# Kernel tuning notes

Measured on AMD Instinct MI355X. Metric: run time of the kernel, lower is better.

The kernel has to match this reference:

```python
import jax, jax.numpy as jnp
import numpy as np

N = 100000
E = 1600000
D_IN, D_HID, D_OUT = 128, 128, 128


def gcn_conv(x, edge_index, W, b):
    """PyG GCNConv with default symmetric normalization and added self-loops.
    out = D^{-1/2} (A + I) D^{-1/2} (x W) + b, edge weights = 1.
    """
    n = x.shape[0]
    h = x @ W                                   # [N, D_out]
    src, dst = edge_index[0], edge_index[1]     # messages flow src -> dst
    ones = jnp.ones(src.shape[0], dtype=x.dtype)
    # degree includes the self-loop (+1), computed on the target index as in PyG
    deg = jax.ops.segment_sum(ones, dst, num_segments=n) + 1.0  # [N]
    dinv = jax.lax.rsqrt(deg)                   # deg >= 1 so safe
    norm = dinv[src] * dinv[dst]                # [E]
    msg = h[src] * norm[:, None]                # [E, D_out]
    agg = jax.ops.segment_sum(msg, dst, num_segments=n)
    # self-loop contribution: norm = dinv_i * dinv_i = 1/deg_i
    out = agg + h * (dinv * dinv)[:, None] + b
    return out


def layer_norm(x, gamma, beta, eps=1e-5):
    mu = jnp.mean(x, axis=-1, keepdims=True)
    var = jnp.mean(jnp.square(x - mu), axis=-1, keepdims=True)
    return (x - mu) * jax.lax.rsqrt(var + eps) * gamma + beta


def setup_inputs() -> dict:
    key = jax.random.key(0)
    ks = jax.random.split(key, 8)
    x = jax.random.normal(ks[0], (N, D_IN), dtype=jnp.float32)
    edge_index = jax.random.randint(ks[1], (2, E), 0, N, dtype=jnp.int64)
    s1 = 1.0 / np.sqrt(D_IN)
    s2 = 1.0 / np.sqrt(D_HID)
    W1 = jax.random.uniform(ks[2], (D_IN, D_HID), jnp.float32, -s1, s1)
    b1 = jnp.zeros((D_HID,), jnp.float32)
    W2 = jax.random.uniform(ks[3], (D_HID, D_OUT), jnp.float32, -s2, s2)
    b2 = jnp.zeros((D_OUT,), jnp.float32)
    gamma = jnp.ones((D_OUT,), jnp.float32)
    beta = jnp.zeros((D_OUT,), jnp.float32)
    return {"x": x, "edge_index": edge_index, "W1": W1, "b1": b1,
            "W2": W2, "b2": b2, "gamma": gamma, "beta": beta}


def reference(x, edge_index, W1, b1, W2, b2, gamma, beta):
    h = gcn_conv(x, edge_index, W1, b1)
    h = jax.nn.relu(h)
    # dropout is identity in eval mode (deterministic reference)
    h = gcn_conv(h, edge_index, W2, b2)
    return layer_norm(h, gamma, beta)
```

## Files before the change

kernel.cpp:

```cpp
#include <hip/hip_runtime.h>


#define N_NODES 100000
#define N_EDGES 1600000
#define NBLK_N  391
#define NB      196
#define BKT_CAP 8960
#define BIN_GRID 391
#define GEMM_GRID 1563
#define MM_GRID  6250

typedef unsigned int  u32;
typedef unsigned short u16;
typedef unsigned char u8;
typedef unsigned long long u64;
typedef __attribute__((ext_vector_type(8))) short bf16x8;
typedef __attribute__((ext_vector_type(4))) float f32x4;

__device__ __forceinline__ float bflo(u32 u){ return __uint_as_float(u << 16); }
__device__ __forceinline__ float bfhi(u32 u){ return __uint_as_float(u & 0xFFFF0000u); }
__device__ __forceinline__ u32 f2b(float f){
  u32 u = __float_as_uint(f);
  return (u + 0x7FFFu + ((u >> 16) & 1u)) >> 16;
}
__device__ __forceinline__ u32 pack2(float a, float b){ return f2b(a) | (f2b(b) << 16); }
__device__ __forceinline__ u32 clampN(int s){
  u32 u = (u32)s;
  return (u < (u32)N_NODES) ? u : (u32)(N_NODES - 1);
}

__global__ __launch_bounds__(64) void detect(const int* __restrict__ ei,
                                             int* __restrict__ flags){
  int l = threadIdx.x;
  int nzodd = (ei[2 * l + 1] != 0) ? 1 : 0;
  #pragma unroll
  for (int o = 32; o > 0; o >>= 1) nzodd += __shfl_xor(nzodd, o, 64);
  if (l == 0) flags[1] = (nzodd == 0) ? 1 : 0;
}


__device__ __forceinline__ void build_wfrag(u16* wfrag, const float* __restrict__ W,
                                            int tid){
  #pragma unroll
  for (int i = 0; i < 8; ++i){
    int fid   = tid + i * 256;
    int lane  = fid & 63;
    int kb    = (fid >> 6) & 3;
    int ntile = fid >> 8;
    int n  = ntile * 16 + (lane & 15);
    int k0 = kb * 32 + (lane >> 4) * 8;
    u16 tmp[8];
    #pragma unroll
    for (int j = 0; j < 8; ++j) tmp[j] = (u16)f2b(W[(k0 + j) * 128 + n]);
    *(bf16x8*)(wfrag + (size_t)fid * 8) = *(const bf16x8*)tmp;
  }
}

__device__ __forceinline__ void gemm_tail(const u16* wfrag, const bf16x8 afrag[4],
                                          int rowbase, int lane,
                                          u16* __restrict__ Hout, int nrows){
  const int m = lane & 15, q = lane >> 4;
  f32x4 acc[8];
  #pragma unroll
  for (int n = 0; n < 8; ++n) acc[n] = (f32x4){0.f, 0.f, 0.f, 0.f};
  #pragma unroll
  for (int n = 0; n < 8; ++n){
    #pragma unroll
    for (int kb = 0; kb < 4; ++kb){
      bf16x8 bfrag = *(const bf16x8*)(wfrag + ((size_t)(n * 4 + kb) * 64 + lane) * 8);
      acc[n] = __builtin_amdgcn_mfma_f32_16x16x32_bf16(afrag[kb], bfrag, acc[n], 0, 0, 0);
    }
  }
  #pragma unroll
  for (int r = 0; r < 4; ++r){
    int orow = rowbase + q * 4 + r;
    if (orow < nrows){
      u16* Or = Hout + (size_t)orow * 128 + m;
      #pragma unroll
      for (int n = 0; n < 8; ++n) Or[n * 16] = (u16)f2b(acc[n][r]);
    }
  }
}

__device__ __forceinline__ void gemm_f32_body(u16* wfrag, const float* __restrict__ A,
                                              const float* __restrict__ W,
                                              u16* __restrict__ Hout, int nrows, int bid){
  build_wfrag(wfrag, W, threadIdx.x);
  __syncthreads();
  const int lane = threadIdx.x & 63;
  const int wv   = threadIdx.x >> 6;
  const int rowbase = bid * 64 + wv * 16;
  const int row  = rowbase + (lane & 15);
  const int rowc = (row < nrows) ? row : (nrows - 1);
  const int q    = lane >> 4;
  bf16x8 afrag[4];
  const float* Ar = A + (size_t)rowc * 128;
  #pragma unroll
  for (int kb = 0; kb < 4; ++kb){
    f32x4 p0 = *(const f32x4*)(Ar + kb * 32 + q * 8);
    f32x4 p1 = *(const f32x4*)(Ar + kb * 32 + q * 8 + 4);
    bf16x8 f;
    f[0] = (short)f2b(p0[0]); f[1] = (short)f2b(p0[1]);
    f[2] = (short)f2b(p0[2]); f[3] = (short)f2b(p0[3]);
    f[4] = (short)f2b(p1[0]); f[5] = (short)f2b(p1[1]);
    f[6] = (short)f2b(p1[2]); f[7] = (short)f2b(p1[3]);
    afrag[kb] = f;
  }
  gemm_tail(wfrag, afrag, rowbase, lane, Hout, nrows);
}


__device__ __forceinline__ void binA_body(u32* cnt ,
                                          const int* __restrict__ ei,
                                          u32* __restrict__ binned,
                                          u32* __restrict__ bucket_fill, int bb){
  u32* gbase = cnt + 256;
  u32* flagp = cnt + 512;
  const int tid = threadIdx.x;
  cnt[tid] = 0;
  if (tid < 64){
    int nz = (ei[2 * tid + 1] != 0) ? 1 : 0;
    u64 b = __ballot(nz);
    if (tid == 0) *flagp = (b == 0ull) ? 1u : 0u;
  }
  __syncthreads();
  const int i64  = (int)*flagp;
  const int base = bb * 4096;
  u32 pk[16], rk[16], bk[16];
  #pragma unroll
  for (int j = 0; j < 16; ++j){
    int e = base + tid + j * 256;
    bk[j] = 0xFFFFFFFFu;
    if (e < N_EDGES){
      int dsti = i64 ? ei[2 * N_EDGES + 2 * e] : ei[N_EDGES + e];
      int srci = i64 ? ei[2 * e]               : ei[e];
      u32 ud = clampN(dsti), us = clampN(srci);
      u32 b = ud >> 9;
      bk[j] = b;
      pk[j] = us | ((ud & 511u) << 17);
      rk[j] = atomicAdd(&cnt[b], 1u);
    }
  }
  __syncthreads();
  u32 c = cnt[tid];
  u32 old = 0;
  if (c) old = atomicAdd(&bucket_fill[tid < NB ? tid : 0], tid < NB ? c : 0u);
  gbase[tid] = old;
  __syncthreads();
  #pragma unroll
  for (int j = 0; j < 16; ++j){
    if (bk[j] != 0xFFFFFFFFu){
      u32 idx = gbase[bk[j]] + rk[j];
      if (idx < BKT_CAP) binned[(size_t)bk[j] * BKT_CAP + idx] = pk[j];
    }
  }
}


__global__ __launch_bounds__(256) void fused_gemm_bin(const float* __restrict__ A,
                                                      const float* __restrict__ W,
                                                      u16* __restrict__ Hout,
                                                      const int* __restrict__ ei,
                                                      u32* __restrict__ binned,
                                                      u32* __restrict__ bucket_fill){
  __shared__ u16 smem[16384];
  if (blockIdx.x < GEMM_GRID){
    gemm_f32_body(smem, A, W, Hout, N_NODES, blockIdx.x);
  } else {
    binA_body((u32*)smem, ei, binned, bucket_fill, blockIdx.x - GEMM_GRID);
  }
}

__global__ __launch_bounds__(256) void gemm_f32in(const float* __restrict__ A,
                                                  const float* __restrict__ W,
                                                  u16* __restrict__ Hout){
  __shared__ u16 smem[16384];
  gemm_f32_body(smem, A, W, Hout, N_NODES, blockIdx.x);
}


__global__ __launch_bounds__(256) void fill_sort(const u32* __restrict__ binned,
                                                 const u32* __restrict__ bucket_fill,
                                                 int* __restrict__ offs,
                                                 float* __restrict__ dinv,
                                                 int* __restrict__ srclist){
  __shared__ u32 cnt[512];
  __shared__ u32 sc[512];
  __shared__ u32 red[256];
  const int b   = blockIdx.x;
  const int tid = threadIdx.x;
  cnt[tid] = 0; cnt[tid + 256] = 0;
  __syncthreads();

  u32 n = bucket_fill[b]; if (n > BKT_CAP) n = BKT_CAP;
  const u32* eb = binned + (size_t)b * BKT_CAP;

  for (u32 i = tid; i < n; i += 256)
    atomicAdd(&cnt[eb[i] >> 17], 1u);

  u32 v = 0;
  if (tid < b && tid < NB){
    u32 f = bucket_fill[tid];
    v = (f > BKT_CAP) ? BKT_CAP : f;
  }
  red[tid] = v;
  __syncthreads();
  for (int o = 128; o > 0; o >>= 1){
    if (tid < o) red[tid] += red[tid + o];
    __syncthreads();
  }
  const u32 base = red[0];
  __syncthreads();

  u32 pair = cnt[2 * tid] + cnt[2 * tid + 1];
  red[tid] = pair;
  __syncthreads();
  for (int o = 1; o < 256; o <<= 1){
    u32 add = (tid >= o) ? red[tid - o] : 0;
    __syncthreads();
    red[tid] += add;
    __syncthreads();
  }
  u32 pex = red[tid] - pair;
  sc[2 * tid]     = pex;
  sc[2 * tid + 1] = pex + cnt[2 * tid];
  __syncthreads();

  const u32 basenode = (u32)b << 9;
  #pragma unroll
  for (int h = 0; h < 2; ++h){
    u32 l = tid + h * 256;
    u32 node = basenode + l;
    if (node < (u32)N_NODES){
      offs[node] = (int)(base + sc[l]);
      dinv[node] = rsqrtf((float)cnt[l] + 1.0f);
    }
  }
  if (b == NB - 1 && tid == 0) offs[N_NODES] = (int)(base + n);

  __syncthreads();
  cnt[tid] = 0; cnt[tid + 256] = 0;
  __syncthreads();
  for (u32 i = tid; i < n; i += 256){
    u32 pk = eb[i];
    u32 d  = pk >> 17;
    u32 r  = atomicAdd(&cnt[d], 1u);
    srclist[base + sc[d] + r] = (int)(pk & 0x1FFFFu);
  }
}


__global__ __launch_bounds__(256) void count_deg(const int* __restrict__ ei,
                                                 const int* __restrict__ flags,
                                                 int* __restrict__ deg){
  int e   = blockIdx.x * 256 + threadIdx.x;
  int i64 = flags[1];
  int dst = i64 ? ei[2 * N_EDGES + 2 * e] : ei[N_EDGES + e];
  if ((unsigned)dst < (unsigned)N_NODES) atomicAdd(&deg[dst], 1);
}

__global__ __launch_bounds__(256) void fill_edges(const int* __restrict__ ei,
                                                  const int* __restrict__ flags,
                                                  int* __restrict__ woff,
                                                  int* __restrict__ srclist){
  int e   = blockIdx.x * 256 + threadIdx.x;
  int i64 = flags[1];
  int dst = i64 ? ei[2 * N_EDGES + 2 * e] : ei[N_EDGES + e];
  int src = i64 ? ei[2 * e]               : ei[e];
  if ((unsigned)dst < (unsigned)N_NODES){
    int p = atomicAdd(&woff[dst], 1);
    if ((unsigned)p < (unsigned)N_EDGES) srclist[p] = clampN(src);
  }
}

__global__ __launch_bounds__(256) void scan1(const int* __restrict__ deg,
                                             int* __restrict__ offs,
                                             int* __restrict__ bsum,
                                             float* __restrict__ dinv){
  __shared__ int sh[256];
  int t = threadIdx.x;
  int i = blockIdx.x * 256 + t;
  int v = (i < N_NODES) ? deg[i] : 0;
  if (i < N_NODES) dinv[i] = rsqrtf((float)v + 1.0f);
  sh[t] = v;
  __syncthreads();
  for (int o = 1; o < 256; o <<= 1){
    int add = (t >= o) ? sh[t - o] : 0;
    __syncthreads();
    sh[t] += add;
    __syncthreads();
  }
  if (i < N_NODES) offs[i] = sh[t] - v;
  if (t == 255)    bsum[blockIdx.x] = sh[255];
}

__global__ __launch_bounds__(512) void scan2(const int* __restrict__ bsum,
                                             int* __restrict__ bofs){
  __shared__ int sh[512];
  int t = threadIdx.x;
  int v = (t < NBLK_N) ? bsum[t] : 0;
  sh[t] = v;
  __syncthreads();
  for (int o = 1; o < 512; o <<= 1){
    int add = (t >= o) ? sh[t - o] : 0;
    __syncthreads();
    sh[t] += add;
    __syncthreads();
  }
  if (t < NBLK_N) bofs[t] = sh[t] - v;
}

__global__ __launch_bounds__(256) void finalize_offs(int* __restrict__ offs,
                                                     const int* __restrict__ bofs,
                                                     int* __restrict__ woff){
  int i = blockIdx.x * 256 + threadIdx.x;
  if (i < N_NODES){
    int o = offs[i] + bofs[blockIdx.x];
    offs[i] = o;
    woff[i] = o;
  }
  if (i == 0) offs[N_NODES] = N_EDGES;
}


#define GATHER_EDGE(sv, A0, A1)                         \
  { u32 s_ = (u32)(sv);                                 \
    float w_ = dinv[s_];                                \
    u32 h_ = H[s_ * 64 + lane];                         \
    A0 = fmaf(w_, bflo(h_), A0);                        \
    A1 = fmaf(w_, bfhi(h_), A1); }

#define GATHER_BODY                                     \
  int beg = offs[node], end = offs[node + 1];           \
  if (end > N_EDGES) end = N_EDGES;                     \
  if (beg < 0 || beg > end) beg = end;                  \
  float a0 = 0.f, a1 = 0.f, c0 = 0.f, c1 = 0.f;         \
  int e = beg;                                          \
  for (; e + 8 <= end; e += 8){                         \
    int s0=srcl[e],s1=srcl[e+1],s2=srcl[e+2],s3=srcl[e+3]; \
    int s4=srcl[e+4],s5=srcl[e+5],s6=srcl[e+6],s7=srcl[e+7]; \
    GATHER_EDGE(s0,a0,a1) GATHER_EDGE(s1,c0,c1)         \
    GATHER_EDGE(s2,a0,a1) GATHER_EDGE(s3,c0,c1)         \
    GATHER_EDGE(s4,a0,a1) GATHER_EDGE(s5,c0,c1)         \
    GATHER_EDGE(s6,a0,a1) GATHER_EDGE(s7,c0,c1)         \
  }                                                     \
  for (; e + 4 <= end; e += 4){                         \
    int s0=srcl[e],s1=srcl[e+1],s2=srcl[e+2],s3=srcl[e+3]; \
    GATHER_EDGE(s0,a0,a1) GATHER_EDGE(s1,c0,c1)         \
    GATHER_EDGE(s2,a0,a1) GATHER_EDGE(s3,c0,c1)         \
  }                                                     \
  for (; e < end; ++e){ int s0=srcl[e]; GATHER_EDGE(s0,a0,a1) } \
  a0 += c0;  a1 += c1;                                  \
  float di = dinv[node];                                \
  u32 hs = H[(u32)node * 64 + lane];                    \
  float v0 = fmaf(a0, di, fmaf(bflo(hs), di * di, bb0)); \
  float v1 = fmaf(a1, di, fmaf(bfhi(hs), di * di, bb1));


__global__ __launch_bounds__(256) void gather_relu_mm(const int* __restrict__ offs,
                                                      const int* __restrict__ srcl,
                                                      const u32* __restrict__ H,
                                                      const float* __restrict__ dinv,
                                                      const float* __restrict__ bias,
                                                      const float* __restrict__ W2,
                                                      u16* __restrict__ H2){
  __shared__ u16 atile[16 * 136];
  const int wv   = threadIdx.x >> 6;
  const int lane = threadIdx.x & 63;
  const int m = lane & 15, q = lane >> 4;
  const int nodebase = blockIdx.x * 16;

  bf16x8 bfragR[2][4];
  {
    const int nn = (wv * 2) * 16 + m;
    const int k0 = q * 8;
    #pragma unroll
    for (int t = 0; t < 2; ++t){
      #pragma unroll
      for (int kb = 0; kb < 4; ++kb){
        bf16x8 f;
        #pragma unroll
        for (int j = 0; j < 8; ++j)
          f[j] = (short)f2b(W2[(kb * 32 + k0 + j) * 128 + nn + t * 16]);
        bfragR[t][kb] = f;
      }
    }
  }

  const float bb0 = bias[2 * lane], bb1 = bias[2 * lane + 1];

  #pragma unroll 1
  for (int j4 = 0; j4 < 4; ++j4){
    const int node = nodebase + wv * 4 + j4;
    GATHER_BODY
    *(u32*)(atile + (size_t)(wv * 4 + j4) * 136 + 2 * lane) =
        pack2(fmaxf(v0, 0.f), fmaxf(v1, 0.f));
  }
  __syncthreads();

  bf16x8 afrag[4];
  #pragma unroll
  for (int kb = 0; kb < 4; ++kb)
    afrag[kb] = *(const bf16x8*)(atile + (size_t)m * 136 + kb * 32 + q * 8);
  f32x4 acc[2];
  acc[0] = (f32x4){0.f, 0.f, 0.f, 0.f};
  acc[1] = (f32x4){0.f, 0.f, 0.f, 0.f};
  #pragma unroll
  for (int t = 0; t < 2; ++t){
    #pragma unroll
    for (int kb = 0; kb < 4; ++kb)
      acc[t] = __builtin_amdgcn_mfma_f32_16x16x32_bf16(afrag[kb], bfragR[t][kb],
                                                       acc[t], 0, 0, 0);
  }
  #pragma unroll
  for (int t = 0; t < 2; ++t){
    const int col = (wv * 2 + t) * 16 + m;
    #pragma unroll
    for (int rr = 0; rr < 4; ++rr){
      const int row = q * 4 + rr;
      H2[(size_t)(nodebase + row) * 128 + col] = (u16)f2b(acc[t][rr]);
    }
  }
}


__global__ __launch_bounds__(256) void gather_ln(const int* __restrict__ offs,
                                                 const int* __restrict__ srcl,
                                                 const u32* __restrict__ H,
                                                 const float* __restrict__ dinv,
                                                 const float* __restrict__ bias,
                                                 const float* __restrict__ gamma,
                                                 const float* __restrict__ beta,
                                                 float* __restrict__ out){
  const int node = blockIdx.x * 4 + (threadIdx.x >> 6);
  const int lane = threadIdx.x & 63;
  const float bb0 = bias[2 * lane], bb1 = bias[2 * lane + 1];
  GATHER_BODY

  float s2 = v0 + v1;
  #pragma unroll
  for (int o = 32; o > 0; o >>= 1) s2 += __shfl_xor(s2, o, 64);
  float mu = s2 * 0.0078125f;
  float d0 = v0 - mu, d1 = v1 - mu;
  float qq = d0 * d0 + d1 * d1;
  #pragma unroll
  for (int o = 32; o > 0; o >>= 1) qq += __shfl_xor(qq, o, 64);
  float rr = rsqrtf(qq * 0.0078125f + 1e-5f);

  float g0 = gamma[2 * lane], g1 = gamma[2 * lane + 1];
  float t0 = beta[2 * lane],  t1 = beta[2 * lane + 1];
  *(float2*)(out + (size_t)node * 128 + 2 * lane) =
      make_float2(fmaf(d0 * rr, g0, t0), fmaf(d1 * rr, g1, t1));
}


extern "C" void kernel_launch(void* const* d_in, const int* in_sizes, int n_in,
                              void* d_out, int out_size, void* d_ws, size_t ws_size,
                              hipStream_t stream){
  const float* x  = (const float*)d_in[0];
  const int*   ei = (const int*)d_in[1];
  const float* W1 = (const float*)d_in[2];
  const float* b1 = (const float*)d_in[3];
  const float* W2 = (const float*)d_in[4];
  const float* b2 = (const float*)d_in[5];
  const float* gm = (const float*)d_in[6];
  const float* bt = (const float*)d_in[7];

  char* ws = (char*)d_ws;
  size_t off = 0;
  auto carve = [&](size_t bytes) -> void* {
    void* p = ws + off;
    off = (off + bytes + 255) & ~(size_t)255;
    return p;
  };
  int*   flags       = (int*)  carve(64);
  u32*   bucket_fill = (u32*)  carve(NB * 4);
  int*   offs        = (int*)  carve((size_t)(N_NODES + 1) * 4);
  float* dinv        = (float*)carve((size_t)N_NODES * 4);
  int*   srclist     = (int*)  carve((size_t)N_EDGES * 4);
  int*   deg         = (int*)  carve((size_t)N_NODES * 4);
  int*   bsum        = (int*)  carve(2048);
  int*   bofs        = (int*)  carve(2048);

  size_t bin_bytes = (size_t)NB * BKT_CAP * 4;
  u32* binned = (u32*)carve(bin_bytes);
  bool use_binned = (ws_size >= off);
  if (!use_binned) off = (size_t)((char*)binned - ws);

  size_t h_bytes = (size_t)N_NODES * 128 * 2;
  u32* H1 = (u32*)d_out;
  u32* H2 = (ws_size >= off + h_bytes) ? (u32*)carve(h_bytes) : (u32*)d_in[0];

  if (use_binned){
    hipMemsetAsync(bucket_fill, 0, NB * 4, stream);
    fused_gemm_bin<<<GEMM_GRID + BIN_GRID, 256, 0, stream>>>(x, W1, (u16*)H1, ei,
                                                             binned, bucket_fill);
    fill_sort     <<<NB, 256, 0, stream>>>(binned, bucket_fill, offs, dinv, srclist);
  } else {
    hipMemsetAsync(deg, 0, (size_t)N_NODES * 4, stream);
    detect        <<<1,             64,  0, stream>>>(ei, flags);
    count_deg     <<<N_EDGES / 256, 256, 0, stream>>>(ei, flags, deg);
    scan1         <<<NBLK_N,        256, 0, stream>>>(deg, offs, bsum, dinv);
    scan2         <<<1,             512, 0, stream>>>(bsum, bofs);
    finalize_offs <<<NBLK_N,        256, 0, stream>>>(offs, bofs, deg );
    fill_edges    <<<N_EDGES / 256, 256, 0, stream>>>(ei, flags, deg , srclist);
    gemm_f32in    <<<GEMM_GRID,     256, 0, stream>>>(x, W1, (u16*)H1);
  }

  gather_relu_mm <<<MM_GRID,     256, 0, stream>>>(offs, srclist, H1, dinv, b1, W2,
                                                   (u16*)H2);
  gather_ln      <<<N_NODES / 4, 256, 0, stream>>>(offs, srclist, H2, dinv, b2, gm, bt,
                                                   (float*)d_out);
}
```

Baseline: 350.4 us.

## Precompute weight fragments once and split layer-2 gather from GEMM

A small prep kernel now converts W1 and W2 into bf16 MFMA fragments once, stored in workspace. It also zeroes the bucket counters, which replaces the memset. The GEMM kernels read the fragments from global memory instead of rebuilding them in shared memory in every block. The fused gather+relu+matmul kernel becomes a plain gather_relu that writes bf16 X2 into the second half of the output buffer, followed by a separate bf16-input GEMM. This avoids each of 6250 blocks converting W2 from fp32 into registers, at the cost of an extra round trip of X2 through memory and one more launch.

```diff
diff --git a/kernel.cpp b/kernel.cpp
--- a/kernel.cpp
+++ b/kernel.cpp
@@ -8,7 +8,6 @@
 #define BKT_CAP 8960
 #define BIN_GRID 391
 #define GEMM_GRID 1563
-#define MM_GRID  6250
 
 typedef unsigned int  u32;
 typedef unsigned short u16;
@@ -39,8 +38,14 @@
 }
 
 
-__device__ __forceinline__ void build_wfrag(u16* wfrag, const float* __restrict__ W,
-                                            int tid){
+__global__ __launch_bounds__(256) void prep_frags(const float* __restrict__ W1,
+                                                  const float* __restrict__ W2,
+                                                  u16* __restrict__ w1f,
+                                                  u16* __restrict__ w2f,
+                                                  u32* __restrict__ bucket_fill){
+  const float* W = blockIdx.x ? W2 : W1;
+  u16* dst = blockIdx.x ? w2f : w1f;
+  const int tid = threadIdx.x;
   #pragma unroll
   for (int i = 0; i < 8; ++i){
     int fid   = tid + i * 256;
@@ -52,11 +57,14 @@
     u16 tmp[8];
     #pragma unroll
     for (int j = 0; j < 8; ++j) tmp[j] = (u16)f2b(W[(k0 + j) * 128 + n]);
-    *(bf16x8*)(wfrag + (size_t)fid * 8) = *(const bf16x8*)tmp;
-  }
-}
-
-__device__ __forceinline__ void gemm_tail(const u16* wfrag, const bf16x8 afrag[4],
+    *(bf16x8*)(dst + (size_t)fid * 8) = *(const bf16x8*)tmp;
+  }
+  if (blockIdx.x == 0 && tid < NB) bucket_fill[tid] = 0;
+}
+
+
+__device__ __forceinline__ void gemm_tail(const u16* __restrict__ wfrag,
+                                          const bf16x8 afrag[4],
                                           int rowbase, int lane,
                                           u16* __restrict__ Hout, int nrows){
   const int m = lane & 15, q = lane >> 4;
@@ -82,11 +90,9 @@
   }
 }
 
-__device__ __forceinline__ void gemm_f32_body(u16* wfrag, const float* __restrict__ A,
-                                              const float* __restrict__ W,
+__device__ __forceinline__ void gemm_f32_body(const u16* __restrict__ wfragG,
+                                              const float* __restrict__ A,
                                               u16* __restrict__ Hout, int nrows, int bid){
-  build_wfrag(wfrag, W, threadIdx.x);
-  __syncthreads();
   const int lane = threadIdx.x & 63;
   const int wv   = threadIdx.x >> 6;
   const int rowbase = bid * 64 + wv * 16;
@@ -106,7 +112,24 @@
     f[6] = (short)f2b(p1[2]); f[7] = (short)f2b(p1[3]);
     afrag[kb] = f;
   }
-  gemm_tail(wfrag, afrag, rowbase, lane, Hout, nrows);
+  gemm_tail(wfragG, afrag, rowbase, lane, Hout, nrows);
+}
+
+__device__ __forceinline__ void gemm_bf16_body(const u16* __restrict__ wfragG,
+                                               const u16* __restrict__ A,
+                                               u16* __restrict__ Hout, int nrows, int bid){
+  const int lane = threadIdx.x & 63;
+  const int wv   = threadIdx.x >> 6;
+  const int rowbase = bid * 64 + wv * 16;
+  const int row  = rowbase + (lane & 15);
+  const int rowc = (row < nrows) ? row : (nrows - 1);
+  const int q    = lane >> 4;
+  bf16x8 afrag[4];
+  const u16* Ar = A + (size_t)rowc * 128;
+  #pragma unroll
+  for (int kb = 0; kb < 4; ++kb)
+    afrag[kb] = *(const bf16x8*)(Ar + kb * 32 + q * 8);
+  gemm_tail(wfragG, afrag, rowbase, lane, Hout, nrows);
 }
 
 
@@ -158,24 +181,28 @@
 
 
 __global__ __launch_bounds__(256) void fused_gemm_bin(const float* __restrict__ A,
-                                                      const float* __restrict__ W,
+                                                      const u16* __restrict__ w1frag,
                                                       u16* __restrict__ Hout,
                                                       const int* __restrict__ ei,
                                                       u32* __restrict__ binned,
                                                       u32* __restrict__ bucket_fill){
-  __shared__ u16 smem[16384];
+  __shared__ u32 binsmem[520];
   if (blockIdx.x < GEMM_GRID){
-    gemm_f32_body(smem, A, W, Hout, N_NODES, blockIdx.x);
+    gemm_f32_body(w1frag, A, Hout, N_NODES, blockIdx.x);
   } else {
-    binA_body((u32*)smem, ei, binned, bucket_fill, blockIdx.x - GEMM_GRID);
+    binA_body(binsmem, ei, binned, bucket_fill, blockIdx.x - GEMM_GRID);
   }
 }
 
 __global__ __launch_bounds__(256) void gemm_f32in(const float* __restrict__ A,
-                                                  const float* __restrict__ W,
+                                                  const u16* __restrict__ wfragG,
                                                   u16* __restrict__ Hout){
-  __shared__ u16 smem[16384];
-  gemm_f32_body(smem, A, W, Hout, N_NODES, blockIdx.x);
+  gemm_f32_body(wfragG, A, Hout, N_NODES, blockIdx.x);
+}
+__global__ __launch_bounds__(256) void gemm_bf16in(const u16* __restrict__ A,
+                                                   const u16* __restrict__ wfragG,
+                                                   u16* __restrict__ Hout){
+  gemm_bf16_body(wfragG, A, Hout, N_NODES, blockIdx.x);
 }
 
 
@@ -356,73 +383,18 @@
   float v0 = fmaf(a0, di, fmaf(bflo(hs), di * di, bb0)); \
   float v1 = fmaf(a1, di, fmaf(bfhi(hs), di * di, bb1));
 
-
-__global__ __launch_bounds__(256) void gather_relu_mm(const int* __restrict__ offs,
-                                                      const int* __restrict__ srcl,
-                                                      const u32* __restrict__ H,
-                                                      const float* __restrict__ dinv,
-                                                      const float* __restrict__ bias,
-                                                      const float* __restrict__ W2,
-                                                      u16* __restrict__ H2){
-  __shared__ u16 atile[16 * 136];
-  const int wv   = threadIdx.x >> 6;
+__global__ __launch_bounds__(256) void gather_relu(const int* __restrict__ offs,
+                                                   const int* __restrict__ srcl,
+                                                   const u32* __restrict__ H,
+                                                   const float* __restrict__ dinv,
+                                                   const float* __restrict__ bias,
+                                                   u32* __restrict__ X2){
+  const int node = blockIdx.x * 4 + (threadIdx.x >> 6);
   const int lane = threadIdx.x & 63;
-  const int m = lane & 15, q = lane >> 4;
-  const int nodebase = blockIdx.x * 16;
-
-  bf16x8 bfragR[2][4];
-  {
-    const int nn = (wv * 2) * 16 + m;
-    const int k0 = q * 8;
-    #pragma unroll
-    for (int t = 0; t < 2; ++t){
-      #pragma unroll
-      for (int kb = 0; kb < 4; ++kb){
-        bf16x8 f;
-        #pragma unroll
-        for (int j = 0; j < 8; ++j)
-          f[j] = (short)f2b(W2[(kb * 32 + k0 + j) * 128 + nn + t * 16]);
-        bfragR[t][kb] = f;
-      }
-    }
-  }
-
   const float bb0 = bias[2 * lane], bb1 = bias[2 * lane + 1];
-
-  #pragma unroll 1
-  for (int j4 = 0; j4 < 4; ++j4){
-    const int node = nodebase + wv * 4 + j4;
-    GATHER_BODY
-    *(u32*)(atile + (size_t)(wv * 4 + j4) * 136 + 2 * lane) =
-        pack2(fmaxf(v0, 0.f), fmaxf(v1, 0.f));
-  }
-  __syncthreads();
-
-  bf16x8 afrag[4];
-  #pragma unroll
-  for (int kb = 0; kb < 4; ++kb)
-    afrag[kb] = *(const bf16x8*)(atile + (size_t)m * 136 + kb * 32 + q * 8);
-  f32x4 acc[2];
-  acc[0] = (f32x4){0.f, 0.f, 0.f, 0.f};
-  acc[1] = (f32x4){0.f, 0.f, 0.f, 0.f};
-  #pragma unroll
-  for (int t = 0; t < 2; ++t){
-    #pragma unroll
-    for (int kb = 0; kb < 4; ++kb)
-      acc[t] = __builtin_amdgcn_mfma_f32_16x16x32_bf16(afrag[kb], bfragR[t][kb],
-                                                       acc[t], 0, 0, 0);
-  }
-  #pragma unroll
-  for (int t = 0; t < 2; ++t){
-    const int col = (wv * 2 + t) * 16 + m;
-    #pragma unroll
-    for (int rr = 0; rr < 4; ++rr){
-      const int row = q * 4 + rr;
-      H2[(size_t)(nodebase + row) * 128 + col] = (u16)f2b(acc[t][rr]);
-    }
-  }
-}
-
+  GATHER_BODY
+  X2[(u32)node * 64 + lane] = pack2(fmaxf(v0, 0.f), fmaxf(v1, 0.f));
+}
 
 __global__ __launch_bounds__(256) void gather_ln(const int* __restrict__ offs,
                                                  const int* __restrict__ srcl,
@@ -474,6 +446,8 @@
     return p;
   };
   int*   flags       = (int*)  carve(64);
+  u16*   w1frag      = (u16*)  carve(128 * 128 * 2);
+  u16*   w2frag      = (u16*)  carve(128 * 128 * 2);
   u32*   bucket_fill = (u32*)  carve(NB * 4);
   int*   offs        = (int*)  carve((size_t)(N_NODES + 1) * 4);
   float* dinv        = (float*)carve((size_t)N_NODES * 4);
@@ -489,11 +463,13 @@
 
   size_t h_bytes = (size_t)N_NODES * 128 * 2;
   u32* H1 = (u32*)d_out;
+  u32* X2 = (u32*)d_out + 6400000;
   u32* H2 = (ws_size >= off + h_bytes) ? (u32*)carve(h_bytes) : (u32*)d_in[0];
 
+  prep_frags <<<2, 256, 0, stream>>>(W1, W2, w1frag, w2frag, bucket_fill);
+
   if (use_binned){
-    hipMemsetAsync(bucket_fill, 0, NB * 4, stream);
-    fused_gemm_bin<<<GEMM_GRID + BIN_GRID, 256, 0, stream>>>(x, W1, (u16*)H1, ei,
+    fused_gemm_bin<<<GEMM_GRID + BIN_GRID, 256, 0, stream>>>(x, w1frag, (u16*)H1, ei,
                                                              binned, bucket_fill);
     fill_sort     <<<NB, 256, 0, stream>>>(binned, bucket_fill, offs, dinv, srclist);
   } else {
@@ -504,11 +480,11 @@
     scan2         <<<1,             512, 0, stream>>>(bsum, bofs);
     finalize_offs <<<NBLK_N,        256, 0, stream>>>(offs, bofs, deg );
     fill_edges    <<<N_EDGES / 256, 256, 0, stream>>>(ei, flags, deg , srclist);
-    gemm_f32in    <<<GEMM_GRID,     256, 0, stream>>>(x, W1, (u16*)H1);
-  }
-
-  gather_relu_mm <<<MM_GRID,     256, 0, stream>>>(offs, srclist, H1, dinv, b1, W2,
-                                                   (u16*)H2);
-  gather_ln      <<<N_NODES / 4, 256, 0, stream>>>(offs, srclist, H2, dinv, b2, gm, bt,
-                                                   (float*)d_out);
-}
+    gemm_f32in    <<<GEMM_GRID,     256, 0, stream>>>(x, w1frag, (u16*)H1);
+  }
+
+  gather_relu <<<N_NODES / 4, 256, 0, stream>>>(offs, srclist, H1, dinv, b1, X2);
+  gemm_bf16in <<<GEMM_GRID,   256, 0, stream>>>((const u16*)X2, w2frag, (u16*)H2);
+  gather_ln   <<<N_NODES / 4, 256, 0, stream>>>(offs, srclist, H2, dinv, b2, gm, bt,
+                                                (float*)d_out);
+}
```

Result: faster. 312.3 us (-10.9%).
